# Optimization experiments

Hardware: AMD Instinct MI355X
Metric: run time of the kernel (lower is better)

## Reference

```python
import jax, jax.numpy as jnp
import numpy as np

# Hard-coded dims from MambaLayer.__init__
D_IN = 20        # input feature dim (Dense infers it; chosen = modelInternalDim)
D_INNER = 20     # modelInternalDim
N_STATES = 10    # modelStates
DT_RANK = 5      # delta_t_rank
BATCH = 4
SEQ = 32768


def setup_inputs() -> dict:
    key = jax.random.key(0)
    ks = jax.random.split(key, 8)
    s = lambda k, shape: jax.random.normal(k, shape, dtype=jnp.float32) * 0.05
    A = jnp.tile(jnp.arange(1, N_STATES + 1, dtype=jnp.float32)[None, :], (D_INNER, 1))
    return {
        "x": jax.random.normal(ks[0], (BATCH, SEQ, D_IN), dtype=jnp.float32),
        "w_in": s(ks[1], (D_IN, 2 * D_INNER)),
        "b_in": jnp.zeros((2 * D_INNER,), jnp.float32),
        "conv_k": s(ks[2], (3, D_INNER, D_INNER)),   # (W, I, O)
        "conv_b": jnp.zeros((D_INNER,), jnp.float32),
        "w_x": s(ks[3], (D_INNER, DT_RANK + 2 * N_STATES)),
        "b_x": jnp.zeros((DT_RANK + 2 * N_STATES,), jnp.float32),
        "w_dt": s(ks[4], (DT_RANK, D_INNER)),
        "b_dt": jnp.zeros((D_INNER,), jnp.float32),
        "A_log": jnp.log(A),
        "D_param": jnp.ones((D_INNER,), jnp.float32),
    }


def _selective_scan(u, delta, A, B, C, D):
    # u, delta: (b,l,d); A: (d,n); B, C: (b,l,n); D: (d,)
    dA = jnp.einsum('bld,dn->bldn', delta, A)                  # (b,l,d,n)
    dB_u = jnp.einsum('bld,bld,bln->bldn', delta, u, B)        # (b,l,d,n)
    # tf.pad(dA[:,1:], [[0,0],[1,1],...])[:,1:] == concat(dA[:,1:], zeros) along l
    dA_shift = jnp.concatenate([dA[:, 1:], jnp.zeros_like(dA[:, :1])], axis=1)
    # reversed cumsum, exponentiate, reverse back
    dA_cumsum = jnp.exp(jnp.flip(jnp.cumsum(jnp.flip(dA_shift, axis=1), axis=1), axis=1))
    x = jnp.cumsum(dB_u * dA_cumsum, axis=1) / (dA_cumsum + 1e-12)
    y = jnp.einsum('bldn,bln->bld', x, C)
    return y + u * D


def reference(x, w_in, b_in, conv_k, conv_b, w_x, b_x, w_dt, b_dt, A_log, D_param):
    # in_projection + split (res half is unused, matching the original call())
    h = x @ w_in + b_in                                        # (b,l,2d)
    h, _res = jnp.split(h, 2, axis=-1)
    # causal Conv1D, kernel_size=3: left-pad by 2
    h = jax.lax.conv_general_dilated(
        h, conv_k, window_strides=(1,), padding=[(2, 0)],
        dimension_numbers=('NWC', 'WIO', 'NWC')) + conv_b
    h = jax.nn.silu(h)                                         # tf.nn.swish
    # ssm
    A = -jnp.exp(A_log)                                        # (d,n)
    xp = h @ w_x + b_x                                         # (b,l,r+2n)
    delta = xp[..., :DT_RANK]
    Bm = xp[..., DT_RANK:DT_RANK + N_STATES]
    Cm = xp[..., DT_RANK + N_STATES:]
    delta = jax.nn.softmax(delta @ w_dt + b_dt, axis=-1)       # (b,l,d)
    return _selective_scan(h, delta, A, Bm, Cm, D_param)
```

## Files before the change

kernel.cpp:

```cpp
#include <hip/hip_runtime.h>
#include <math.h>

#define B_   4
#define L_   32768
#define DI   20
#define NS   10
#define TBLK 128
#define NCB  256

#define OFF_AP  0u
#define OFF_RS  204800u
#define OFF_SC  409600u
#define OFF_TOT 430080u
#define OFF_H16 430160u
#define HD  0u
#define HU  2621440u
#define HB  5242880u
#define HC  6553600u

typedef _Float16 h16;
typedef _Float16 half8 __attribute__((ext_vector_type(8)));
typedef _Float16 half4 __attribute__((ext_vector_type(4)));
typedef float f32x4 __attribute__((ext_vector_type(4)));

template<int CTRL>
__device__ __forceinline__ float dppf(float idv, float src) {
    union U { float f; int i; };
    U o, s, r; o.f = idv; s.f = src;
    r.i = __builtin_amdgcn_update_dpp(o.i, s.i, CTRL, 0xf, 0xf, false);
    return r.f;
}
#define ROW_SHR1 0x111
#define ROW_SHR2 0x112
#define ROW_SHR4 0x114
#define ROW_SHR8 0x118

#define OPSCAN16(Ac, Bc) \
    { float aP = dppf<ROW_SHR1>(1.0f, Ac); float bP = dppf<ROW_SHR1>(0.0f, Bc); \
      Bc = fmaf(Ac, bP, Bc); Ac *= aP; \
      aP = dppf<ROW_SHR2>(1.0f, Ac); bP = dppf<ROW_SHR2>(0.0f, Bc); \
      Bc = fmaf(Ac, bP, Bc); Ac *= aP; \
      aP = dppf<ROW_SHR4>(1.0f, Ac); bP = dppf<ROW_SHR4>(0.0f, Bc); \
      Bc = fmaf(Ac, bP, Bc); Ac *= aP; \
      aP = dppf<ROW_SHR8>(1.0f, Ac); bP = dppf<ROW_SHR8>(0.0f, Bc); \
      Bc = fmaf(Ac, bP, Bc); Ac *= aP; }

#define SUMSCAN16(v) \
    { v += dppf<ROW_SHR1>(0.0f, v); v += dppf<ROW_SHR2>(0.0f, v); \
      v += dppf<ROW_SHR4>(0.0f, v); v += dppf<ROW_SHR8>(0.0f, v); }

#define XS_   0
#define WST   2864
#define MT_   2864
#define UL_   0
#define XP5_  4608
#define DS__  0
#define CS_   2720
#define BS_   5440
#define WX_   6800
#define WDTo  7800
#define BDTo  7900
#define BXo   7920
#define POOLH 7948

__global__ __launch_bounds__(320) void k1(
    const float* __restrict__ x, const float* __restrict__ w_in,
    const float* __restrict__ b_in, const float* __restrict__ conv_k,
    const float* __restrict__ conv_b, const float* __restrict__ w_x,
    const float* __restrict__ b_x, const float* __restrict__ w_dt,
    const float* __restrict__ b_dt, const float* __restrict__ A_log,
    h16* __restrict__ dh, h16* __restrict__ uh,
    h16* __restrict__ Bh, h16* __restrict__ Ch,
    float* __restrict__ ap_ws, float* __restrict__ rs_ws, float* __restrict__ sc_ws)
{
    __shared__ __align__(16) h16 P[POOLH];
    __shared__ float beff_s[20];

    const int tid = threadIdx.x;
    const int c   = blockIdx.x;
    const int b   = blockIdx.y;
    const int l0  = c * TBLK;

    for (int i = tid; i < 400;  i += 320) P[WST + i]       = (h16)w_in[(i/20)*40 + (i%20)];
    for (int i = tid; i < 1200; i += 320) P[WST + 400 + i] = (h16)conv_k[i];
    for (int i = tid; i < 1000; i += 320) {
        int j = i / 40, k = i - j*40;
        P[WX_ + i] = (k < 20) ? (h16)w_x[k*25 + j] : (h16)0.0f;
    }
    for (int i = tid; i < 100; i += 320) P[WDTo + i] = (h16)w_dt[i];
    if (tid < 20) P[BDTo + tid] = (h16)b_dt[tid];
    if (tid < 25) P[BXo  + tid] = (h16)b_x[tid];
    for (int idx = tid; idx < 130*20; idx += 320) {
        int p = idx / 20, i = idx - p*20;
        int l = l0 - 2 + p;
        P[XS_ + p*22 + i] = (l >= 0) ? (h16)x[((size_t)b*L_ + l)*DI + i] : (h16)0.0f;
    }
    __syncthreads();

    float me[4]; int mei[4];
    #pragma unroll
    for (int r = 0; r < 4; r++) {
        int e = tid + r*320;
        float acc = 0.0f;
        if (e < 1200) {
            int cc = e / 20, o = e - cc*20;
            int w = cc / 20, i = cc - w*20;
            #pragma unroll
            for (int op = 0; op < 20; op++)
                acc = fmaf((float)P[WST + i*20 + op],
                           (float)P[WST + 400 + (w*20 + op)*20 + o], acc);
        }
        me[r] = acc; mei[r] = e;
    }
    float be = 0.0f;
    if (tid < 20) {
        be = conv_b[tid];
        #pragma unroll
        for (int w = 0; w < 3; w++)
            #pragma unroll
            for (int op = 0; op < 20; op++)
                be = fmaf(b_in[op], (float)P[WST + 400 + (w*20 + op)*20 + tid], be);
    }
    __syncthreads();
    #pragma unroll
    for (int r = 0; r < 4; r++) {
        int e = mei[r];
        if (e < 1200) {
            int cc = e / 20, o = e - cc*20;
            P[MT_ + o*68 + cc] = (h16)me[r];
        }
    }
    if (tid < 20) beff_s[tid] = be;
    __syncthreads();

    const int wv  = tid >> 6;
    const int ln  = tid & 63;
    const int m16 = ln & 15;
    const int q   = ln >> 4;
    float uval[4][4];
    if (wv < 4) {
        #pragma unroll
        for (int jj = 0; jj < 4; jj++) {
            int job = wv*4 + jj, mt = job >> 1, nt = job & 1;
            int t_row = mt*16 + m16;
            int dcol  = nt*16 + m16;
            int dmin  = dcol < 20 ? dcol : 19;
            f32x4 acc = {0.0f, 0.0f, 0.0f, 0.0f};
            #pragma unroll
            for (int kh = 0; kh < 2; kh++) {
                half8 af;
                #pragma unroll
                for (int j = 0; j < 8; j++) {
                    int k = kh*32 + (q<<3) + j;
                    int w = (k >= 20) + (k >= 40);
                    int i = k - 20*w;
                    af[j] = (k < 60) ? P[XS_ + (t_row + w)*22 + i] : (h16)0.0f;
                }
                half8 bf;
                *(half4*)&bf    = *(const half4*)&P[MT_ + dmin*68 + kh*32 + (q<<3)];
                *((half4*)&bf+1)= *(const half4*)&P[MT_ + dmin*68 + kh*32 + (q<<3) + 4];
                acc = __builtin_amdgcn_mfma_f32_16x16x32_f16(af, bf, acc, 0, 0, 0);
            }
            float bf2 = beff_s[dmin];
            #pragma unroll
            for (int r = 0; r < 4; r++) {
                float a = acc[r] + bf2;
                uval[jj][r] = a / (1.0f + __expf(-a));
            }
        }
    }
    __syncthreads();
    if (wv < 4) {
        #pragma unroll
        for (int jj = 0; jj < 4; jj++) {
            int job = wv*4 + jj, mt = job >> 1, nt = job & 1;
            int dcol = nt*16 + m16;
            if (dcol < 20) {
                #pragma unroll
                for (int r = 0; r < 4; r++)
                    P[UL_ + (mt*16 + q*4 + r)*36 + dcol] = (h16)uval[jj][r];
            }
        }
    }
    for (int i = tid; i < 128*12; i += 320) {
        int t = i / 12, z = i - t*12;
        P[UL_ + t*36 + 20 + z] = (h16)0.0f;
    }
    __syncthreads();

    float xv[4][4];
    if (wv < 4) {
        #pragma unroll
        for (int jj = 0; jj < 4; jj++) {
            int job = wv*4 + jj, mt = job >> 1, nt = job & 1;
            int t_row = mt*16 + m16;
            int j     = nt*16 + m16;
            int jmin  = j < 25 ? j : 24;
            f32x4 acc = {0.0f, 0.0f, 0.0f, 0.0f};
            half8 af;
            *(half4*)&af     = *(const half4*)&P[UL_ + t_row*36 + (q<<3)];
            *((half4*)&af+1) = *(const half4*)&P[UL_ + t_row*36 + (q<<3) + 4];
            half8 bf = *(const half8*)&P[WX_ + jmin*40 + (q<<3)];
            acc = __builtin_amdgcn_mfma_f32_16x16x32_f16(af, bf, acc, 0, 0, 0);
            float bx = (j < 25) ? (float)P[BXo + j] : 0.0f;
            #pragma unroll
            for (int r = 0; r < 4; r++) xv[jj][r] = acc[r] + bx;
        }
        #pragma unroll
        for (int jj = 0; jj < 4; jj++) {
            int job = wv*4 + jj, nt = job & 1, mt = job >> 1;
            int j = nt*16 + m16;
            #pragma unroll
            for (int r = 0; r < 4; r++) {
                int t_out = mt*16 + q*4 + r;
                if (j < 5)            P[XP5_ + t_out*5 + j]        = (h16)xv[jj][r];
                else if (j < 15)      P[BS_ + (j - 5)*136 + t_out] = (h16)xv[jj][r];
            }
        }
    }
    __syncthreads();

    const int d  = tid >> 4;
    const int s  = tid & 15;
    const int bd = b*DI + d;

    float u8[8];
    #pragma unroll
    for (int j = 0; j < 8; j++) u8[j] = (float)P[UL_ + (8*s + j)*36 + d];

    float dl[20];
    if (tid < 128) {
        const int t = tid;
        #pragma unroll
        for (int d2 = 0; d2 < 20; d2++)
            uh[(size_t)(b*DI + d2)*L_ + l0 + t] = P[UL_ + t*36 + d2];
        #pragma unroll
        for (int n = 0; n < NS; n++)
            Bh[(size_t)(b*NS + n)*L_ + l0 + t] = P[BS_ + n*136 + t];
        float xq[5];
        #pragma unroll
        for (int r = 0; r < 5; r++) xq[r] = (float)P[XP5_ + t*5 + r];
        #pragma unroll
        for (int d2 = 0; d2 < 20; d2++) dl[d2] = (float)P[BDTo + d2];
        #pragma unroll
        for (int r = 0; r < 5; r++) {
            float dv = xq[r];
            #pragma unroll
            for (int d2 = 0; d2 < 20; d2++)
                dl[d2] = fmaf(dv, (float)P[WDTo + r*20 + d2], dl[d2]);
        }
        float mx = dl[0];
        #pragma unroll
        for (int d2 = 1; d2 < 20; d2++) mx = fmaxf(mx, dl[d2]);
        float sm = 0.0f;
        #pragma unroll
        for (int d2 = 0; d2 < 20; d2++) { dl[d2] = __expf(dl[d2] - mx); sm += dl[d2]; }
        float inv = 1.0f / sm;
        #pragma unroll
        for (int d2 = 0; d2 < 20; d2++) dl[d2] *= inv;
    }
    __syncthreads();

    if (tid < 128) {
        const int t = tid;
        #pragma unroll
        for (int d2 = 0; d2 < 20; d2++) {
            h16 dlh = (h16)dl[d2];
            P[DS__ + d2*136 + t] = dlh;
            dh[(size_t)(b*DI + d2)*L_ + l0 + t] = dlh;
        }
    }
    if (wv < 4) {
        #pragma unroll
        for (int jj = 0; jj < 4; jj++) {
            int job = wv*4 + jj, nt = job & 1, mt = job >> 1;
            int j = nt*16 + m16;
            if (j >= 15 && j < 25) {
                #pragma unroll
                for (int r = 0; r < 4; r++)
                    P[CS_ + (j - 15)*136 + (mt*16 + q*4 + r)] = (h16)xv[jj][r];
            }
        }
    }
    __syncthreads();

    if (tid < 128) {
        const int t = tid;
        #pragma unroll
        for (int n = 0; n < NS; n++)
            Ch[(size_t)(b*NS + n)*L_ + l0 + t] = P[CS_ + n*136 + t];
    }
    float d8[8], du8[8];
    { half8 hv = *(const half8*)&P[DS__ + d*136 + 8*s];
      #pragma unroll
      for (int j = 0; j < 8; j++) d8[j] = (float)hv[j]; }
    #pragma unroll
    for (int j = 0; j < 8; j++) du8[j] = d8[j]*u8[j];

    float ssum = 0.0f;
    #pragma unroll
    for (int j = 0; j < 8; j++) ssum += d8[j];
    SUMSCAN16(ssum);
    if (s == 15) sc_ws[(size_t)bd*NCB + c] = ssum;

    float A_dn[NS];
    #pragma unroll
    for (int n = 0; n < NS; n++) A_dn[n] = -__expf(A_log[d*NS + n]);

    #pragma unroll 1
    for (int n = 0; n < NS; n++) {
        half8 bv = *(const half8*)&P[BS_ + n*136 + 8*s];
        float Ac = 1.0f, Bc = 0.0f;
        #pragma unroll
        for (int j = 0; j < 8; j++) {
            float a = __expf(A_dn[n]*d8[j]);
            Bc = fmaf(a, Bc, du8[j]*(float)bv[j]);
            Ac *= a;
        }
        OPSCAN16(Ac, Bc);
        if (s == 15) {
            size_t o = ((size_t)bd*NS + n)*NCB + c;
            ap_ws[o] = Ac;
            rs_ws[o] = Bc;
        }
    }
}

__global__ __launch_bounds__(64) void kC2(
    const float* __restrict__ ap_ws, float* __restrict__ rs_ws,
    float* __restrict__ sc_ws, float* __restrict__ tot_ws)
{
    const int bd   = blockIdx.x;
    const int lane = threadIdx.x;
    const size_t sb = (size_t)bd*NCB + lane*4;

    float4 sv = *(const float4*)(sc_ws + sb);
    float l1 = sv.x, l2 = l1 + sv.y, l3 = l2 + sv.z, l4 = l3 + sv.w;
    float inc = l4;
    #pragma unroll
    for (int off = 1; off < 64; off <<= 1) {
        float t = __shfl_up(inc, off);
        if (lane >= off) inc += t;
    }
    float ex = __shfl_up(inc, 1);
    if (lane == 0) ex = 0.0f;
    *(float4*)(sc_ws + sb) = make_float4(ex, ex + l1, ex + l2, ex + l3);
    if (lane == 63) tot_ws[bd] = inc;

    #pragma unroll 1
    for (int n = 0; n < NS; n++) {
        const size_t base = ((size_t)bd*NS + n)*NCB + lane*4;
        float4 av = *(const float4*)(ap_ws + base);
        float4 rv = *(const float4*)(rs_ws + base);
        float Ac = av.x, Bc = rv.x;
        Bc = fmaf(av.y, Bc, rv.y); Ac *= av.y;
        Bc = fmaf(av.z, Bc, rv.z); Ac *= av.z;
        Bc = fmaf(av.w, Bc, rv.w); Ac *= av.w;
        #pragma unroll
        for (int off = 1; off < 64; off <<= 1) {
            float aP = __shfl_up(Ac, off);
            float bP = __shfl_up(Bc, off);
            if (lane >= off) { Bc = fmaf(Ac, bP, Bc); Ac *= aP; }
        }
        float pB = __shfl_up(Bc, 1);
        if (lane == 0) pB = 0.0f;
        float r  = pB;
        float o0 = r; r = fmaf(av.x, r, rv.x);
        float o1 = r; r = fmaf(av.y, r, rv.y);
        float o2 = r; r = fmaf(av.z, r, rv.z);
        float o3 = r;
        *(float4*)(rs_ws + base) = make_float4(o0, o1, o2, o3);
    }
}

__global__ __launch_bounds__(320) void kD(
    const h16* __restrict__ dh, const h16* __restrict__ uh,
    const h16* __restrict__ Bh, const h16* __restrict__ Ch,
    const float* __restrict__ A_log, const float* __restrict__ D_param,
    const float* __restrict__ rs_ws, const float* __restrict__ sc_ws,
    const float* __restrict__ tot_ws, float* __restrict__ out)
{
    __shared__ float ylT[20*132];
    const int tid = threadIdx.x;
    const int d   = tid >> 4;
    const int s   = tid & 15;
    const int c   = blockIdx.x;
    const int b   = blockIdx.y;
    const int bd  = b*DI + d;
    const size_t t0 = (size_t)c*TBLK + s*8;

    const float Tot = tot_ws[bd];
    float A_dn[NS];
    float Amax = -1e30f;
    #pragma unroll
    for (int n = 0; n < NS; n++) {
        A_dn[n] = -__expf(A_log[d*NS + n]);
        Amax = fmaxf(Amax, A_dn[n]);
    }
    const float pref_end = (c + 1 < NCB) ? sc_ws[(size_t)bd*NCB + c + 1] : Tot;
    const bool active = fmaf(Amax, Tot - pref_end, 40.0f) > 0.0f;

    float u8[8];
    { half8 hv = *(const half8*)(uh + (size_t)bd*L_ + t0);
      #pragma unroll
      for (int j = 0; j < 8; j++) u8[j] = (float)hv[j]; }
    const float Dd = D_param[d];
    float yv[8];
    #pragma unroll
    for (int j = 0; j < 8; j++) yv[j] = u8[j]*Dd;

    if (active) {
        float d8[8], du8[8];
        { half8 hv = *(const half8*)(dh + (size_t)bd*L_ + t0);
          #pragma unroll
          for (int j = 0; j < 8; j++) d8[j] = (float)hv[j]; }
        #pragma unroll
        for (int j = 0; j < 8; j++) du8[j] = d8[j]*u8[j];

        float lp[8];
        { float run = 0.0f;
          #pragma unroll
          for (int j = 0; j < 8; j++) { run += d8[j]; lp[j] = run; } }
        float inc = lp[7];
        SUMSCAN16(inc);
        float ex = dppf<ROW_SHR1>(0.0f, inc);
        const float basep = sc_ws[(size_t)bd*NCB + c] + ex;

        float rin[NS];
        #pragma unroll
        for (int n = 0; n < NS; n++) rin[n] = rs_ws[((size_t)bd*NS + n)*NCB + c];

        float yacc[8];
        #pragma unroll
        for (int j = 0; j < 8; j++) yacc[j] = 0.0f;

        half8 bv0 = *(const half8*)(Bh + (size_t)(b*NS + 0)*L_ + t0);
        half8 cv0 = *(const half8*)(Ch + (size_t)(b*NS + 0)*L_ + t0);
        half8 bv1 = *(const half8*)(Bh + (size_t)(b*NS + 1)*L_ + t0);
        half8 cv1 = *(const half8*)(Ch + (size_t)(b*NS + 1)*L_ + t0);

        #pragma unroll 1
        for (int n = 0; n < NS; n++) {
            half8 bv = bv0, cv = cv0;
            bv0 = bv1; cv0 = cv1;
            if (n + 2 < NS) {
                bv1 = *(const half8*)(Bh + (size_t)(b*NS + n + 2)*L_ + t0);
                cv1 = *(const half8*)(Ch + (size_t)(b*NS + n + 2)*L_ + t0);
            }
            float a8[8], b8[8];
            #pragma unroll
            for (int j = 0; j < 8; j++) {
                a8[j] = __expf(A_dn[n]*d8[j]);
                b8[j] = du8[j]*(float)bv[j];
            }
            float Ac = 1.0f, Bc = 0.0f;
            #pragma unroll
            for (int j = 0; j < 8; j++) { Bc = fmaf(a8[j], Bc, b8[j]); Ac *= a8[j]; }
            OPSCAN16(Ac, Bc);
            float pA = dppf<ROW_SHR1>(1.0f, Ac);
            float pB = dppf<ROW_SHR1>(0.0f, Bc);
            float r  = fmaf(pA, rin[n], pB);

            float G[8];
            G[7] = __expf(A_dn[n]*(Tot - (basep + lp[7])));
            #pragma unroll
            for (int j = 6; j >= 0; j--) G[j] = G[j+1]*a8[j+1];
            #pragma unroll
            for (int j = 0; j < 8; j++) {
                r = fmaf(a8[j], r, b8[j]);
                float damp = G[j] * __builtin_amdgcn_rcpf(G[j] + 1e-12f);
                yacc[j] = fmaf((float)cv[j]*damp, r, yacc[j]);
            }
        }
        #pragma unroll
        for (int j = 0; j < 8; j++) yv[j] = fmaf(u8[j], Dd, yacc[j]);
    }

    *(float4*)&ylT[d*132 + 8*s]     = *(float4*)(yv);
    *(float4*)&ylT[d*132 + 8*s + 4] = *(float4*)(yv + 4);
    __syncthreads();

    float4* ob4 = (float4*)(out + ((size_t)b*L_ + (size_t)c*TBLK)*DI);
    for (int i = tid; i < TBLK*DI/4; i += 320) {
        int t = i / 5, qq = (i - t*5)*4;
        ob4[i] = make_float4(ylT[qq*132 + t], ylT[(qq+1)*132 + t],
                             ylT[(qq+2)*132 + t], ylT[(qq+3)*132 + t]);
    }
}

extern "C" void kernel_launch(void* const* d_in, const int* in_sizes, int n_in,
                              void* d_out, int out_size, void* d_ws, size_t ws_size,
                              hipStream_t stream) {
    const float* x      = (const float*)d_in[0];
    const float* w_in   = (const float*)d_in[1];
    const float* b_in   = (const float*)d_in[2];
    const float* conv_k = (const float*)d_in[3];
    const float* conv_b = (const float*)d_in[4];
    const float* w_x    = (const float*)d_in[5];
    const float* b_x    = (const float*)d_in[6];
    const float* w_dt   = (const float*)d_in[7];
    const float* b_dt   = (const float*)d_in[8];
    const float* A_log  = (const float*)d_in[9];
    const float* D_par  = (const float*)d_in[10];
    float* out = (float*)d_out;
    float* ws  = (float*)d_ws;

    float* ap_ws  = ws + OFF_AP;
    float* rs_ws  = ws + OFF_RS;
    float* sc_ws  = ws + OFF_SC;
    float* tot_ws = ws + OFF_TOT;
    h16*   hbase  = (h16*)(ws + OFF_H16);
    h16* dh = hbase + HD;
    h16* uh = hbase + HU;
    h16* Bh = hbase + HB;
    h16* Ch = hbase + HC;

    k1<<<dim3(NCB, B_), 320, 0, stream>>>(x, w_in, b_in, conv_k, conv_b,
                                          w_x, b_x, w_dt, b_dt, A_log,
                                          dh, uh, Bh, Ch,
                                          ap_ws, rs_ws, sc_ws);
    kC2<<<B_*DI, 64, 0, stream>>>(ap_ws, rs_ws, sc_ws, tot_ws);
    kD<<<dim3(NCB, B_), 320, 0, stream>>>(dh, uh, Bh, Ch, A_log, D_par,
                                          rs_ws, sc_ws, tot_ws, out);
}
```

Measured before the change: 130.9 us.

## Precompute fused in-proj/conv weights in a separate kernel and streamline k1 staging

Adds a single-block kernel k0 that folds the input projection into the conv weights, along with the other fp16 weight copies and the fused bias, and writes them once to workspace. Each k1 block previously recomputed these itself; now it just copies them into shared memory. k1 also loads x with float2 vector reads into an unpadded row layout that MFMA A-fragments read as half4, writes C straight to global from registers, precomputes delta*u in shared memory, and uses rcp intrinsics. The cost is an extra kernel launch, a serial dependency on k0, and some extra rounding from fp16 storage of delta*u.

```diff
diff --git a/kernel.cpp b/kernel.cpp
--- a/kernel.cpp
+++ b/kernel.cpp
@@ -8,15 +8,22 @@
 #define TBLK 128
 #define NCB  256
 
-#define OFF_AP  0u
-#define OFF_RS  204800u
-#define OFF_SC  409600u
-#define OFF_TOT 430080u
-#define OFF_H16 430160u
+#define OFF_AP   0u
+#define OFF_RS   204800u
+#define OFF_SC   409600u
+#define OFF_TOT  430080u
+#define OFF_BEFF 430160u
+#define OFF_H16  430192u
 #define HD  0u
 #define HU  2621440u
 #define HB  5242880u
 #define HC  6553600u
+#define HW  7864320u
+#define WMT 0
+#define WWX 1440
+#define WWD 2440
+#define WBD 2540
+#define WBX 2560
 
 typedef _Float16 h16;
 typedef _Float16 half8 __attribute__((ext_vector_type(8)));
@@ -50,25 +57,64 @@
       v += dppf<ROW_SHR4>(0.0f, v); v += dppf<ROW_SHR8>(0.0f, v); }
 
 #define XS_   0
-#define WST   2864
-#define MT_   2864
+#define MT_   2640
 #define UL_   0
+#define DS__  0
+#define DUS_  2720
 #define XP5_  4608
-#define DS__  0
-#define CS_   2720
-#define BS_   5440
-#define WX_   6800
-#define WDTo  7800
-#define BDTo  7900
-#define BXo   7920
-#define POOLH 7948
+#define BS_   5448
+#define WXo   6808
+#define WDTo  7808
+#define BDTo  7908
+#define BXo   7928
+#define POOLH 7956
+
+__global__ __launch_bounds__(320) void k0(
+    const float* __restrict__ w_in, const float* __restrict__ b_in,
+    const float* __restrict__ conv_k, const float* __restrict__ conv_b,
+    const float* __restrict__ w_x, const float* __restrict__ w_dt,
+    const float* __restrict__ b_dt, const float* __restrict__ b_x,
+    h16* __restrict__ wts, float* __restrict__ beff)
+{
+    __shared__ float W[1600];
+    const int tid = threadIdx.x;
+    for (int i = tid; i < 400;  i += 320) W[i]       = w_in[(i/20)*40 + (i%20)];
+    for (int i = tid; i < 1200; i += 320) W[400 + i] = conv_k[i];
+    __syncthreads();
+    for (int e = tid; e < 1200; e += 320) {
+        int cc = e/20, o = e - cc*20;
+        int w = cc/20, i = cc - w*20;
+        float acc = 0.0f;
+        #pragma unroll
+        for (int op = 0; op < 20; op++)
+            acc = fmaf(W[i*20 + op], W[400 + (w*20 + op)*20 + o], acc);
+        wts[WMT + o*72 + cc] = (h16)acc;
+    }
+    for (int i = tid; i < 240; i += 320) {
+        int o = i/12, cc = 60 + (i - (i/12)*12);
+        wts[WMT + o*72 + cc] = (h16)0.0f;
+    }
+    for (int i = tid; i < 1000; i += 320) {
+        int j = i/40, k = i - j*40;
+        wts[WWX + i] = (k < 20) ? (h16)w_x[k*25 + j] : (h16)0.0f;
+    }
+    for (int i = tid; i < 100; i += 320) wts[WWD + i] = (h16)w_dt[i];
+    if (tid < 20) wts[WBD + tid] = (h16)b_dt[tid];
+    if (tid < 25) wts[WBX + tid] = (h16)b_x[tid];
+    if (tid < 20) {
+        float be = conv_b[tid];
+        #pragma unroll
+        for (int w = 0; w < 3; w++)
+            #pragma unroll
+            for (int op = 0; op < 20; op++)
+                be = fmaf(b_in[op], W[400 + (w*20 + op)*20 + tid], be);
+        beff[tid] = be;
+    }
+}
 
 __global__ __launch_bounds__(320) void k1(
-    const float* __restrict__ x, const float* __restrict__ w_in,
-    const float* __restrict__ b_in, const float* __restrict__ conv_k,
-    const float* __restrict__ conv_b, const float* __restrict__ w_x,
-    const float* __restrict__ b_x, const float* __restrict__ w_dt,
-    const float* __restrict__ b_dt, const float* __restrict__ A_log,
+    const float* __restrict__ x, const h16* __restrict__ wts,
+    const float* __restrict__ beff, const float* __restrict__ A_log,
     h16* __restrict__ dh, h16* __restrict__ uh,
     h16* __restrict__ Bh, h16* __restrict__ Ch,
     float* __restrict__ ap_ws, float* __restrict__ rs_ws, float* __restrict__ sc_ws)
@@ -81,56 +127,26 @@
     const int b   = blockIdx.y;
     const int l0  = c * TBLK;
 
-    for (int i = tid; i < 400;  i += 320) P[WST + i]       = (h16)w_in[(i/20)*40 + (i%20)];
-    for (int i = tid; i < 1200; i += 320) P[WST + 400 + i] = (h16)conv_k[i];
-    for (int i = tid; i < 1000; i += 320) {
-        int j = i / 40, k = i - j*40;
-        P[WX_ + i] = (k < 20) ? (h16)w_x[k*25 + j] : (h16)0.0f;
-    }
-    for (int i = tid; i < 100; i += 320) P[WDTo + i] = (h16)w_dt[i];
-    if (tid < 20) P[BDTo + tid] = (h16)b_dt[tid];
-    if (tid < 25) P[BXo  + tid] = (h16)b_x[tid];
-    for (int idx = tid; idx < 130*20; idx += 320) {
-        int p = idx / 20, i = idx - p*20;
-        int l = l0 - 2 + p;
-        P[XS_ + p*22 + i] = (l >= 0) ? (h16)x[((size_t)b*L_ + l)*DI + i] : (h16)0.0f;
-    }
-    __syncthreads();
-
-    float me[4]; int mei[4];
-    #pragma unroll
-    for (int r = 0; r < 4; r++) {
-        int e = tid + r*320;
-        float acc = 0.0f;
-        if (e < 1200) {
-            int cc = e / 20, o = e - cc*20;
-            int w = cc / 20, i = cc - w*20;
-            #pragma unroll
-            for (int op = 0; op < 20; op++)
-                acc = fmaf((float)P[WST + i*20 + op],
-                           (float)P[WST + 400 + (w*20 + op)*20 + o], acc);
-        }
-        me[r] = acc; mei[r] = e;
-    }
-    float be = 0.0f;
-    if (tid < 20) {
-        be = conv_b[tid];
-        #pragma unroll
-        for (int w = 0; w < 3; w++)
-            #pragma unroll
-            for (int op = 0; op < 20; op++)
-                be = fmaf(b_in[op], (float)P[WST + 400 + (w*20 + op)*20 + tid], be);
-    }
-    __syncthreads();
-    #pragma unroll
-    for (int r = 0; r < 4; r++) {
-        int e = mei[r];
-        if (e < 1200) {
-            int cc = e / 20, o = e - cc*20;
-            P[MT_ + o*68 + cc] = (h16)me[r];
-        }
-    }
-    if (tid < 20) beff_s[tid] = be;
+    {
+        const int* src = (const int*)(wts + WMT);
+        int* dst = (int*)&P[MT_];
+        for (int i = tid; i < 720; i += 320) dst[i] = src[i];
+        const int* s2 = (const int*)(wts + WWX);
+        int* d2 = (int*)&P[WXo];
+        for (int i = tid; i < 572; i += 320) d2[i] = s2[i];
+        if (tid == 0) P[WXo + 1144] = wts[WWX + 1144];
+        if (tid < 20) beff_s[tid] = beff[tid];
+    }
+    {
+        const float* xb = x + ((size_t)b*L_ + l0)*DI - 2*DI;
+        for (int i = tid; i < 1320; i += 320) {
+            float2 v;
+            if (i >= 1300 || (c == 0 && i < 20)) v = make_float2(0.0f, 0.0f);
+            else v = *(const float2*)(xb + 2*i);
+            P[XS_ + 2*i]     = (h16)v.x;
+            P[XS_ + 2*i + 1] = (h16)v.y;
+        }
+    }
     __syncthreads();
 
     const int wv  = tid >> 6;
@@ -148,28 +164,25 @@
             f32x4 acc = {0.0f, 0.0f, 0.0f, 0.0f};
             #pragma unroll
             for (int kh = 0; kh < 2; kh++) {
-                half8 af;
-                #pragma unroll
-                for (int j = 0; j < 8; j++) {
-                    int k = kh*32 + (q<<3) + j;
-                    int w = (k >= 20) + (k >= 40);
-                    int i = k - 20*w;
-                    af[j] = (k < 60) ? P[XS_ + (t_row + w)*22 + i] : (h16)0.0f;
-                }
-                half8 bf;
-                *(half4*)&bf    = *(const half4*)&P[MT_ + dmin*68 + kh*32 + (q<<3)];
-                *((half4*)&bf+1)= *(const half4*)&P[MT_ + dmin*68 + kh*32 + (q<<3) + 4];
+                half8 af, bf;
+                int ab = XS_ + t_row*20 + kh*32 + (q<<3);
+                *(half4*)&af         = *(const half4*)&P[ab];
+                *(((half4*)&af) + 1) = *(const half4*)&P[ab + 4];
+                int bb = MT_ + dmin*72 + kh*32 + (q<<3);
+                *(half4*)&bf         = *(const half4*)&P[bb];
+                *(((half4*)&bf) + 1) = *(const half4*)&P[bb + 4];
                 acc = __builtin_amdgcn_mfma_f32_16x16x32_f16(af, bf, acc, 0, 0, 0);
             }
-            float bf2 = beff_s[dmin];
+            float bfv = beff_s[dmin];
             #pragma unroll
             for (int r = 0; r < 4; r++) {
-                float a = acc[r] + bf2;
-                uval[jj][r] = a / (1.0f + __expf(-a));
-            }
-        }
-    }
-    __syncthreads();
+                float a = acc[r] + bfv;
+                uval[jj][r] = a * __builtin_amdgcn_rcpf(1.0f + __expf(-a));
+            }
+        }
+    }
+    __syncthreads();
+
     if (wv < 4) {
         #pragma unroll
         for (int jj = 0; jj < 4; jj++) {
@@ -182,8 +195,8 @@
             }
         }
     }
-    for (int i = tid; i < 128*12; i += 320) {
-        int t = i / 12, z = i - t*12;
+    for (int i = tid; i < 1536; i += 320) {
+        int t = i/12, z = i - t*12;
         P[UL_ + t*36 + 20 + z] = (h16)0.0f;
     }
     __syncthreads();
@@ -197,10 +210,13 @@
             int j     = nt*16 + m16;
             int jmin  = j < 25 ? j : 24;
             f32x4 acc = {0.0f, 0.0f, 0.0f, 0.0f};
-            half8 af;
-            *(half4*)&af     = *(const half4*)&P[UL_ + t_row*36 + (q<<3)];
-            *((half4*)&af+1) = *(const half4*)&P[UL_ + t_row*36 + (q<<3) + 4];
-            half8 bf = *(const half8*)&P[WX_ + jmin*40 + (q<<3)];
+            half8 af, bf;
+            int ab = UL_ + t_row*36 + (q<<3);
+            *(half4*)&af         = *(const half4*)&P[ab];
+            *(((half4*)&af) + 1) = *(const half4*)&P[ab + 4];
+            int bb = WXo + jmin*40 + (q<<3);
+            *(half4*)&bf         = *(const half4*)&P[bb];
+            *(((half4*)&bf) + 1) = *(const half4*)&P[bb + 4];
             acc = __builtin_amdgcn_mfma_f32_16x16x32_f16(af, bf, acc, 0, 0, 0);
             float bx = (j < 25) ? (float)P[BXo + j] : 0.0f;
             #pragma unroll
@@ -208,14 +224,67 @@
         }
         #pragma unroll
         for (int jj = 0; jj < 4; jj++) {
-            int job = wv*4 + jj, nt = job & 1, mt = job >> 1;
+            int job = wv*4 + jj, mt = job >> 1, nt = job & 1;
             int j = nt*16 + m16;
             #pragma unroll
             for (int r = 0; r < 4; r++) {
-                int t_out = mt*16 + q*4 + r;
-                if (j < 5)            P[XP5_ + t_out*5 + j]        = (h16)xv[jj][r];
-                else if (j < 15)      P[BS_ + (j - 5)*136 + t_out] = (h16)xv[jj][r];
-            }
+                int t = mt*16 + q*4 + r;
+                h16 hv = (h16)xv[jj][r];
+                if (j < 5)       P[XP5_ + t*5 + j] = hv;
+                else if (j < 15) P[BS_ + (j - 5)*136 + t] = hv;
+                else if (j < 25) Ch[(size_t)(b*NS + (j - 15))*L_ + l0 + t] = hv;
+            }
+        }
+    }
+    __syncthreads();
+
+    h16 urow[20];
+    float dl[20];
+    if (tid < 128) {
+        const int t = tid;
+        *(half4*)&urow[0]  = *(const half4*)&P[UL_ + t*36 + 0];
+        *(half4*)&urow[4]  = *(const half4*)&P[UL_ + t*36 + 4];
+        *(half4*)&urow[8]  = *(const half4*)&P[UL_ + t*36 + 8];
+        *(half4*)&urow[12] = *(const half4*)&P[UL_ + t*36 + 12];
+        *(half4*)&urow[16] = *(const half4*)&P[UL_ + t*36 + 16];
+        #pragma unroll
+        for (int d2 = 0; d2 < 20; d2++)
+            uh[(size_t)(b*DI + d2)*L_ + l0 + t] = urow[d2];
+        #pragma unroll
+        for (int n = 0; n < NS; n++)
+            Bh[(size_t)(b*NS + n)*L_ + l0 + t] = P[BS_ + n*136 + t];
+        float xq[5];
+        #pragma unroll
+        for (int r = 0; r < 5; r++) xq[r] = (float)P[XP5_ + t*5 + r];
+        #pragma unroll
+        for (int d2 = 0; d2 < 20; d2++) dl[d2] = (float)P[BDTo + d2];
+        #pragma unroll
+        for (int r = 0; r < 5; r++) {
+            float dv = xq[r];
+            #pragma unroll
+            for (int d2 = 0; d2 < 20; d2++)
+                dl[d2] = fmaf(dv, (float)P[WDTo + r*20 + d2], dl[d2]);
+        }
+        float mx = dl[0];
+        #pragma unroll
+        for (int d2 = 1; d2 < 20; d2++) mx = fmaxf(mx, dl[d2]);
+        float sm = 0.0f;
+        #pragma unroll
+        for (int d2 = 0; d2 < 20; d2++) { dl[d2] = __expf(dl[d2] - mx); sm += dl[d2]; }
+        float inv = __builtin_amdgcn_rcpf(sm);
+        #pragma unroll
+        for (int d2 = 0; d2 < 20; d2++) dl[d2] *= inv;
+    }
+    __syncthreads();
+
+    if (tid < 128) {
+        const int t = tid;
+        #pragma unroll
+        for (int d2 = 0; d2 < 20; d2++) {
+            h16 dlh = (h16)dl[d2];
+            P[DS__ + d2*136 + t] = dlh;
+            P[DUS_ + d2*136 + t] = (h16)((float)dlh * (float)urow[d2]);
+            dh[(size_t)(b*DI + d2)*L_ + l0 + t] = dlh;
         }
     }
     __syncthreads();
@@ -224,78 +293,13 @@
     const int s  = tid & 15;
     const int bd = b*DI + d;
 
-    float u8[8];
-    #pragma unroll
-    for (int j = 0; j < 8; j++) u8[j] = (float)P[UL_ + (8*s + j)*36 + d];
-
-    float dl[20];
-    if (tid < 128) {
-        const int t = tid;
-        #pragma unroll
-        for (int d2 = 0; d2 < 20; d2++)
-            uh[(size_t)(b*DI + d2)*L_ + l0 + t] = P[UL_ + t*36 + d2];
-        #pragma unroll
-        for (int n = 0; n < NS; n++)
-            Bh[(size_t)(b*NS + n)*L_ + l0 + t] = P[BS_ + n*136 + t];
-        float xq[5];
-        #pragma unroll
-        for (int r = 0; r < 5; r++) xq[r] = (float)P[XP5_ + t*5 + r];
-        #pragma unroll
-        for (int d2 = 0; d2 < 20; d2++) dl[d2] = (float)P[BDTo + d2];
-        #pragma unroll
-        for (int r = 0; r < 5; r++) {
-            float dv = xq[r];
-            #pragma unroll
-            for (int d2 = 0; d2 < 20; d2++)
-                dl[d2] = fmaf(dv, (float)P[WDTo + r*20 + d2], dl[d2]);
-        }
-        float mx = dl[0];
-        #pragma unroll
-        for (int d2 = 1; d2 < 20; d2++) mx = fmaxf(mx, dl[d2]);
-        float sm = 0.0f;
-        #pragma unroll
-        for (int d2 = 0; d2 < 20; d2++) { dl[d2] = __expf(dl[d2] - mx); sm += dl[d2]; }
-        float inv = 1.0f / sm;
-        #pragma unroll
-        for (int d2 = 0; d2 < 20; d2++) dl[d2] *= inv;
-    }
-    __syncthreads();
-
-    if (tid < 128) {
-        const int t = tid;
-        #pragma unroll
-        for (int d2 = 0; d2 < 20; d2++) {
-            h16 dlh = (h16)dl[d2];
-            P[DS__ + d2*136 + t] = dlh;
-            dh[(size_t)(b*DI + d2)*L_ + l0 + t] = dlh;
-        }
-    }
-    if (wv < 4) {
-        #pragma unroll
-        for (int jj = 0; jj < 4; jj++) {
-            int job = wv*4 + jj, nt = job & 1, mt = job >> 1;
-            int j = nt*16 + m16;
-            if (j >= 15 && j < 25) {
-                #pragma unroll
-                for (int r = 0; r < 4; r++)
-                    P[CS_ + (j - 15)*136 + (mt*16 + q*4 + r)] = (h16)xv[jj][r];
-            }
-        }
-    }
-    __syncthreads();
-
-    if (tid < 128) {
-        const int t = tid;
-        #pragma unroll
-        for (int n = 0; n < NS; n++)
-            Ch[(size_t)(b*NS + n)*L_ + l0 + t] = P[CS_ + n*136 + t];
-    }
     float d8[8], du8[8];
     { half8 hv = *(const half8*)&P[DS__ + d*136 + 8*s];
       #pragma unroll
       for (int j = 0; j < 8; j++) d8[j] = (float)hv[j]; }
-    #pragma unroll
-    for (int j = 0; j < 8; j++) du8[j] = d8[j]*u8[j];
+    { half8 hv = *(const half8*)&P[DUS_ + d*136 + 8*s];
+      #pragma unroll
+      for (int j = 0; j < 8; j++) du8[j] = (float)hv[j]; }
 
     float ssum = 0.0f;
     #pragma unroll
@@ -509,14 +513,17 @@
     float* rs_ws  = ws + OFF_RS;
     float* sc_ws  = ws + OFF_SC;
     float* tot_ws = ws + OFF_TOT;
+    float* beff   = ws + OFF_BEFF;
     h16*   hbase  = (h16*)(ws + OFF_H16);
-    h16* dh = hbase + HD;
-    h16* uh = hbase + HU;
-    h16* Bh = hbase + HB;
-    h16* Ch = hbase + HC;
-
-    k1<<<dim3(NCB, B_), 320, 0, stream>>>(x, w_in, b_in, conv_k, conv_b,
-                                          w_x, b_x, w_dt, b_dt, A_log,
+    h16* dh  = hbase + HD;
+    h16* uh  = hbase + HU;
+    h16* Bh  = hbase + HB;
+    h16* Ch  = hbase + HC;
+    h16* wts = hbase + HW;
+
+    k0<<<1, 320, 0, stream>>>(w_in, b_in, conv_k, conv_b, w_x, w_dt, b_dt, b_x,
+                              wts, beff);
+    k1<<<dim3(NCB, B_), 320, 0, stream>>>(x, wts, beff, A_log,
                                           dh, uh, Bh, Ch,
                                           ap_ws, rs_ws, sc_ws);
     kC2<<<B_*DI, 64, 0, stream>>>(ap_ws, rs_ws, sc_ws, tot_ws);
```

Result: faster. 125.0 us (-4.5%).
